# Optimization experiments

Hardware: AMD Instinct MI355X
Metric: run time of the kernel (lower is better)

The kernel has to match this reference:

```python
import jax, jax.numpy as jnp
import numpy as np

THRESHOLD = 0.5  # args.threshold: mask prob >= threshold means 'read' this token
HIDDEN = 256
EMBED = 300
BATCH = 64
STEPS = 2048


def setup_inputs() -> dict:
    key = jax.random.key(0)
    ks = jax.random.split(key, 10)
    H, E = HIDDEN, EMBED
    s = 1.0 / np.sqrt(H)
    return {
        "embedded": jax.random.normal(ks[0], (BATCH, STEPS, E), dtype=jnp.float32),
        "mask": jax.random.uniform(ks[1], (BATCH, STEPS), dtype=jnp.float32),
        "lengths": jax.random.randint(ks[2], (BATCH,), 1, STEPS + 1),
        # LSTM cell params (torch gate order i, f, g, o)
        "W_ih": jax.random.uniform(ks[3], (4 * H, E), minval=-s, maxval=s, dtype=jnp.float32),
        "W_hh": jax.random.uniform(ks[4], (4 * H, H), minval=-s, maxval=s, dtype=jnp.float32),
        "b_ih": jax.random.uniform(ks[5], (4 * H,), minval=-s, maxval=s, dtype=jnp.float32),
        "b_hh": jax.random.uniform(ks[6], (4 * H,), minval=-s, maxval=s, dtype=jnp.float32),
        "W_out": jax.random.uniform(ks[7], (2, H), minval=-s, maxval=s, dtype=jnp.float32),
        "b_out": jax.random.uniform(ks[8], (2,), minval=-s, maxval=s, dtype=jnp.float32),
    }


def reference(embedded, mask, lengths, W_ih, W_hh, b_ih, b_hh, W_out, b_out):
    B, T, E = embedded.shape
    H = W_hh.shape[1]
    b = b_ih + b_hh

    def step(carry, xs):
        h, c = carry
        x_t, m_t = xs  # [B,E], [B]
        z = x_t @ W_ih.T + h @ W_hh.T + b  # [B,4H]
        i, f, g, o = jnp.split(z, 4, axis=-1)
        i = jax.nn.sigmoid(i)
        f = jax.nn.sigmoid(f)
        g = jnp.tanh(g)
        o = jax.nn.sigmoid(o)
        c_new = f * c + i * g
        h_new = o * jnp.tanh(c_new)
        read = (m_t >= THRESHOLD)[:, None]  # skip-RNN gate
        h2 = jnp.where(read, h_new, h)
        c2 = jnp.where(read, c_new, c)
        return (h2, c2), h2

    h0 = jnp.zeros((B, H), embedded.dtype)
    c0 = jnp.zeros((B, H), embedded.dtype)
    xs = (jnp.swapaxes(embedded, 0, 1), mask.T)  # time-major
    _, hs = jax.lax.scan(step, (h0, c0), xs)  # hs: [T,B,H]

    idx = jnp.clip(lengths - 1, 0, T - 1)
    last = hs[idx, jnp.arange(B)]  # [B,H] last relevant output
    logits = last @ W_out.T + b_out
    probs = jax.nn.softmax(logits, axis=-1)
    predictions = jnp.argmax(probs, axis=1)
    return probs, predictions
```

## Files before the change

### kernel.cpp

```cpp
#include <hip/hip_runtime.h>
#include <math.h>

#define BATCH  64
#define TSTEPS 2048
#define EMBED  300
#define HID    256
#define GATES  1024
#define WSTRIDE 34
#define ASTR   328

typedef __fp16 h2 __attribute__((ext_vector_type(2)));
typedef __fp16 h4 __attribute__((ext_vector_type(4)));
typedef __fp16 h8 __attribute__((ext_vector_type(8)));
typedef float  f4 __attribute__((ext_vector_type(4)));

__device__ __forceinline__ h2 pack_h2(float a, float b) {
    return __builtin_amdgcn_cvt_pkrtz(a, b);
}
__device__ __forceinline__ h2 bc_h2(unsigned u) {
    return __builtin_bit_cast(h2, u);
}
__device__ __forceinline__ float dot2f(h2 w, h2 h, float acc) {
#if __has_builtin(__builtin_amdgcn_fdot2)
    return __builtin_amdgcn_fdot2(w, h, acc, false);
#else
    return acc + (float)w[0]*(float)h[0] + (float)w[1]*(float)h[1];
#endif
}
__device__ __forceinline__ float rcpf_(float x) {
#if __has_builtin(__builtin_amdgcn_rcpf)
    return __builtin_amdgcn_rcpf(x);
#else
    return 1.0f / x;
#endif
}
__device__ __forceinline__ float sigm_(float x) { return rcpf_(1.f + __expf(-x)); }
__device__ __forceinline__ float tanh_(float x) { return 1.f - 2.f*rcpf_(__expf(2.f*x) + 1.f); }

__global__ __launch_bounds__(256) void k_compact(
    const float* __restrict__ mask, const int* __restrict__ lengths,
    int* __restrict__ list, int* __restrict__ cnt,
    float* __restrict__ h_state, float* __restrict__ c_state,
    int t0, int CT, int first_chunk)
{
    int b = blockIdx.x, tid = threadIdx.x;
    if (first_chunk) {
        h_state[b*HID + tid] = 0.f;
        c_state[b*HID + tid] = 0.f;
    }
    int idx = lengths[b] - 1;
    idx = idx < 0 ? 0 : (idx > TSTEPS-1 ? TSTEPS-1 : idx);

    __shared__ int wcnt[4];
    __shared__ int running;
    if (tid == 0) running = 0;
    __syncthreads();

    for (int base = 0; base < CT; base += 256) {
        int t = t0 + base + tid;
        bool pred = ((base + tid) < CT) && (t <= idx)
                    && (mask[b*TSTEPS + t] >= 0.5f);
        unsigned long long bal = __ballot(pred);
        int wave = tid >> 6, lane = tid & 63;
        if (lane == 0) wcnt[wave] = __popcll(bal);
        __syncthreads();
        int off = running;
        for (int w2 = 0; w2 < wave; ++w2) off += wcnt[w2];
        off += __popcll(bal & ((1ull << lane) - 1ull));
        if (pred) list[b*CT + off] = t;
        __syncthreads();
        if (tid == 0) running += wcnt[0] + wcnt[1] + wcnt[2] + wcnt[3];
        __syncthreads();
    }
    if (tid == 0) cnt[b] = running;
}

__global__ __launch_bounds__(256) void k_gemm(
    const float* __restrict__ emb, const float* __restrict__ W_ih,
    const int* __restrict__ list, const int* __restrict__ cnt,
    float* __restrict__ Z, int CT)
{
    int b = blockIdx.z;
    int mb = cnt[b];
    int n0 = blockIdx.x * 128;
    int tid = threadIdx.x;
    int w = tid >> 6, l = tid & 63;

    __shared__ _Float16 Al[64 * ASTR];
    __shared__ _Float16 Bl[128 * ASTR];
    __shared__ int tl[64];

    for (int idx = tid; idx < 128*75; idx += 256) {
        int r = idx / 75, c = idx - 75*r;
        float4 v = ((const float4*)(W_ih + (size_t)(n0 + r)*EMBED))[c];
        *(h2*)&Bl[r*ASTR + 4*c]     = pack_h2(v.x, v.y);
        *(h2*)&Bl[r*ASTR + 4*c + 2] = pack_h2(v.z, v.w);
    }
    for (int idx = tid; idx < 128*14; idx += 256) {
        int r = idx / 14, c2 = idx - 14*r;
        *(unsigned*)&Bl[r*ASTR + 300 + 2*c2] = 0u;
    }
    for (int idx = tid; idx < 64*14; idx += 256) {
        int r = idx / 14, c2 = idx - 14*r;
        *(unsigned*)&Al[r*ASTR + 300 + 2*c2] = 0u;
    }

    int arow = w*16 + (l & 15);
    int kg4  = (l >> 4) * 4;
    int drow0 = w*16 + (l >> 4)*4;

    for (int i0 = 0; i0 < mb; i0 += 64) {
        __syncthreads();
        if (tid < 64) {
            int j = i0 + tid;
            tl[tid] = (j < mb) ? list[b*CT + j] : -1;
        }
        __syncthreads();
        for (int idx = tid; idx < 64*75; idx += 256) {
            int r = idx / 75, c = idx - 75*r;
            float4 v = {0.f, 0.f, 0.f, 0.f};
            int trow = tl[r];
            if (trow >= 0)
                v = ((const float4*)(emb + ((size_t)b*TSTEPS + trow)*EMBED))[c];
            *(h2*)&Al[r*ASTR + 4*c]     = pack_h2(v.x, v.y);
            *(h2*)&Al[r*ASTR + 4*c + 2] = pack_h2(v.z, v.w);
        }
        __syncthreads();

        f4 acc[8];
        #pragma unroll
        for (int nt = 0; nt < 8; ++nt) acc[nt] = f4{0.f, 0.f, 0.f, 0.f};

        #pragma unroll 2
        for (int ks = 0; ks < 10; ++ks) {
            int kb = ks*32 + kg4;
            h4 alo = *(const h4*)&Al[arow*ASTR + kb];
            h4 ahi = *(const h4*)&Al[arow*ASTR + kb + 16];
            h8 af = __builtin_shufflevector(alo, ahi, 0,1,2,3,4,5,6,7);
            #pragma unroll
            for (int nt = 0; nt < 8; ++nt) {
                int brow = nt*16 + (l & 15);
                h4 blo = *(const h4*)&Bl[brow*ASTR + kb];
                h4 bhi = *(const h4*)&Bl[brow*ASTR + kb + 16];
                h8 bf = __builtin_shufflevector(blo, bhi, 0,1,2,3,4,5,6,7);
                acc[nt] = __builtin_amdgcn_mfma_f32_16x16x32_f16(af, bf, acc[nt], 0, 0, 0);
            }
        }

        #pragma unroll
        for (int nt = 0; nt < 8; ++nt) {
            #pragma unroll
            for (int j = 0; j < 4; ++j) {
                int r = drow0 + j;
                if (i0 + r < mb)
                    Z[((size_t)b*CT + i0 + r)*GATES + n0 + nt*16 + (l & 15)] = acc[nt][j];
            }
        }
    }
}

__global__ __launch_bounds__(1024, 1) void k_lstm(
    const float* __restrict__ Z, const int* __restrict__ cnt,
    const float* __restrict__ W_hh,
    const float* __restrict__ b_ih, const float* __restrict__ b_hh,
    float* __restrict__ h_state, float* __restrict__ c_state, int CT)
{
    int b = blockIdx.x;
    int tid = threadIdx.x;
    int d   = tid & 255;
    int g   = tid >> 8;

    __shared__ unsigned wlds[1024 * WSTRIDE];
    __shared__ float act3[3][256];
    __shared__ __align__(16) _Float16 h_arr[HID];

    for (int idx = tid; idx < 1024*32; idx += 1024) {
        int r = idx >> 5, k = idx & 31;
        float2 v = ((const float2*)(W_hh + (size_t)r*HID))[k];
        *(h2*)&wlds[r*WSTRIDE + k] = pack_h2(v.x, v.y);
    }
    h2 wr[96];
    {
        const float2* pw = (const float2*)(W_hh + (size_t)tid*HID);
        #pragma unroll
        for (int t = 0; t < 96; ++t) {
            float2 v = pw[32 + t];
            wr[t] = pack_h2(v.x, v.y);
        }
    }
    float bias = b_ih[tid] + b_hh[tid];

    float c_reg = 0.f;
    if (tid < 256) {
        h_arr[d] = (_Float16)h_state[(size_t)b*HID + d];
        c_reg    = c_state[(size_t)b*HID + d];
    }
    __syncthreads();

    int mb = cnt[b];
    float zcur = (mb > 0) ? Z[((size_t)b*CT)*GATES + tid] : 0.f;

    for (int j = 0; j < mb; ++j) {
        float znext = (j + 1 < mb) ? Z[((size_t)b*CT + j + 1)*GATES + tid] : 0.f;

        float a0 = 0.f, a1 = 0.f;
        #pragma unroll
        for (int c = 0; c < 32; ++c) {
            uint4 hv = ((const uint4*)h_arr)[c];
            h2 h0 = bc_h2(hv.x), h1 = bc_h2(hv.y);
            h2 hx = bc_h2(hv.z), h3 = bc_h2(hv.w);
            h2 w0, w1, w2, w3;
            if (c < 8) {
                uint2 q01 = *(const uint2*)&wlds[tid*WSTRIDE + 4*c];
                uint2 q23 = *(const uint2*)&wlds[tid*WSTRIDE + 4*c + 2];
                w0 = bc_h2(q01.x); w1 = bc_h2(q01.y);
                w2 = bc_h2(q23.x); w3 = bc_h2(q23.y);
            } else {
                int t = (c - 8) * 4;
                w0 = wr[t+0]; w1 = wr[t+1]; w2 = wr[t+2]; w3 = wr[t+3];
            }
            a0 = dot2f(w0, h0, a0);
            a1 = dot2f(w1, h1, a1);
            a0 = dot2f(w2, hx, a0);
            a1 = dot2f(w3, h3, a1);
        }
        float a = zcur + bias + (a0 + a1);
        float v = (g == 2) ? tanh_(a) : sigm_(a);
        if (g) act3[g-1][d] = v;
        __syncthreads();

        if (tid < 256) {
            float fv = act3[0][d], gv = act3[1][d], ov = act3[2][d];
            c_reg = fv * c_reg + v * gv;
            float hn = ov * tanh_(c_reg);
            h_arr[d] = (_Float16)hn;
        }
        __syncthreads();
        zcur = znext;
    }

    if (tid < 256) {
        h_state[(size_t)b*HID + d] = (float)h_arr[d];
        c_state[(size_t)b*HID + d] = c_reg;
    }
}

__global__ __launch_bounds__(64) void k_final(
    const float* __restrict__ h_state, const float* __restrict__ W_out,
    const float* __restrict__ b_out, float* __restrict__ out)
{
    int b = threadIdx.x;
    float l0 = b_out[0], l1 = b_out[1];
    for (int k = 0; k < HID; ++k) {
        float h = h_state[b*HID + k];
        l0 += h * W_out[k];
        l1 += h * W_out[HID + k];
    }
    float m  = fmaxf(l0, l1);
    float e0 = expf(l0 - m), e1 = expf(l1 - m);
    float s  = e0 + e1;
    float p0 = e0 / s, p1 = e1 / s;
    out[b*2 + 0] = p0;
    out[b*2 + 1] = p1;
    out[BATCH*2 + b] = (p1 > p0) ? 1.0f : 0.0f;
}

extern "C" void kernel_launch(void* const* d_in, const int* in_sizes, int n_in,
                              void* d_out, int out_size, void* d_ws, size_t ws_size,
                              hipStream_t stream)
{
    (void)in_sizes; (void)n_in; (void)out_size;
    const float* emb   = (const float*)d_in[0];
    const float* mask  = (const float*)d_in[1];
    const int*   len   = (const int*)  d_in[2];
    const float* W_ih  = (const float*)d_in[3];
    const float* W_hh  = (const float*)d_in[4];
    const float* b_ih  = (const float*)d_in[5];
    const float* b_hh  = (const float*)d_in[6];
    const float* W_out = (const float*)d_in[7];
    const float* b_out = (const float*)d_in[8];
    float* out = (float*)d_out;

    char* p = (char*)d_ws;
    auto carve = [&](size_t bytes) -> char* {
        char* r = p;
        p += (bytes + 255) & ~(size_t)255;
        return r;
    };
    float* h_state = (float*)carve((size_t)BATCH*HID*4);
    float* c_state = (float*)carve((size_t)BATCH*HID*4);
    int*   cntb    = (int*)  carve((size_t)BATCH*4);

    size_t fixed = (size_t)(p - (char*)d_ws);
    int CT = TSTEPS;
    while (CT > 64) {
        size_t lb = (((size_t)BATCH*CT*4) + 255) & ~(size_t)255;
        size_t zb = (size_t)BATCH*CT*GATES*4;
        if (fixed + lb + zb + 1024 <= ws_size) break;
        CT >>= 1;
    }
    int*   list = (int*)  carve((size_t)BATCH*CT*4);
    float* Z    = (float*)carve((size_t)BATCH*CT*GATES*4);

    int nchunks = TSTEPS / CT;
    for (int c = 0; c < nchunks; ++c) {
        int t0 = c * CT;
        int first = (c == 0) ? 1 : 0;
        hipLaunchKernelGGL(k_compact, dim3(BATCH), dim3(256), 0, stream,
                           mask, len, list, cntb, h_state, c_state,
                           t0, CT, first);
        hipLaunchKernelGGL(k_gemm, dim3(8, 1, BATCH), dim3(256), 0, stream,
                           emb, W_ih, list, cntb, Z, CT);
        hipLaunchKernelGGL(k_lstm, dim3(BATCH), dim3(1024), 0, stream,
                           Z, cntb, W_hh, b_ih, b_hh,
                           h_state, c_state, CT);
    }
    hipLaunchKernelGGL(k_final, dim3(1), dim3(64), 0, stream,
                       h_state, W_out, b_out, out);
}
```

Baseline: 2.579 ms.

## Compute LSTM recurrent matvec with MFMA using register-resident W_hh fragments

The recurrent h·W_hh product in the per-batch LSTM kernel now runs as MFMA 16x16x32 f16 instructions instead of per-thread fdot2 loops. The whole fp16 W_hh slice is held in registers as MFMA B-fragments, and only row 0 of the A operand carries h (other lanes are masked to zero). The block shrinks from 1024 to 512 threads, and the 256 cell threads each apply all four gates, removing the separate activation exchange array. Most of each MFMA's work is wasted on zero rows, and holding 64 h8 fragments per thread puts heavy pressure on registers.

After: 4.995 ms. 93.7% more time.

```diff
diff --git a/kernel.cpp b/kernel.cpp
--- a/kernel.cpp
+++ b/kernel.cpp
@@ -6,7 +6,6 @@
 #define EMBED  300
 #define HID    256
 #define GATES  1024
-#define WSTRIDE 34
 #define ASTR   328
 
 typedef __fp16 h2 __attribute__((ext_vector_type(2)));
@@ -17,15 +16,8 @@
 __device__ __forceinline__ h2 pack_h2(float a, float b) {
     return __builtin_amdgcn_cvt_pkrtz(a, b);
 }
-__device__ __forceinline__ h2 bc_h2(unsigned u) {
-    return __builtin_bit_cast(h2, u);
-}
-__device__ __forceinline__ float dot2f(h2 w, h2 h, float acc) {
-#if __has_builtin(__builtin_amdgcn_fdot2)
-    return __builtin_amdgcn_fdot2(w, h, acc, false);
-#else
-    return acc + (float)w[0]*(float)h[0] + (float)w[1]*(float)h[1];
-#endif
+__device__ __forceinline__ unsigned pack_u(float a, float b) {
+    return __builtin_bit_cast(unsigned, __builtin_amdgcn_cvt_pkrtz(a, b));
 }
 __device__ __forceinline__ float rcpf_(float x) {
 #if __has_builtin(__builtin_amdgcn_rcpf)
@@ -93,8 +85,8 @@
     for (int idx = tid; idx < 128*75; idx += 256) {
         int r = idx / 75, c = idx - 75*r;
         float4 v = ((const float4*)(W_ih + (size_t)(n0 + r)*EMBED))[c];
-        *(h2*)&Bl[r*ASTR + 4*c]     = pack_h2(v.x, v.y);
-        *(h2*)&Bl[r*ASTR + 4*c + 2] = pack_h2(v.z, v.w);
+        *(unsigned*)&Bl[r*ASTR + 4*c]     = pack_u(v.x, v.y);
+        *(unsigned*)&Bl[r*ASTR + 4*c + 2] = pack_u(v.z, v.w);
     }
     for (int idx = tid; idx < 128*14; idx += 256) {
         int r = idx / 14, c2 = idx - 14*r;
@@ -122,8 +114,8 @@
             int trow = tl[r];
             if (trow >= 0)
                 v = ((const float4*)(emb + ((size_t)b*TSTEPS + trow)*EMBED))[c];
-            *(h2*)&Al[r*ASTR + 4*c]     = pack_h2(v.x, v.y);
-            *(h2*)&Al[r*ASTR + 4*c + 2] = pack_h2(v.z, v.w);
+            *(unsigned*)&Al[r*ASTR + 4*c]     = pack_u(v.x, v.y);
+            *(unsigned*)&Al[r*ASTR + 4*c + 2] = pack_u(v.z, v.w);
         }
         __syncthreads();
 
@@ -159,84 +151,103 @@
     }
 }
 
-__global__ __launch_bounds__(1024, 1) void k_lstm(
+__global__ __launch_bounds__(512) void k_lstm(
     const float* __restrict__ Z, const int* __restrict__ cnt,
     const float* __restrict__ W_hh,
     const float* __restrict__ b_ih, const float* __restrict__ b_hh,
     float* __restrict__ h_state, float* __restrict__ c_state, int CT)
 {
-    int b = blockIdx.x;
+    int b   = blockIdx.x;
     int tid = threadIdx.x;
+    int w   = tid >> 6;
+    int l   = tid & 63;
+    int g   = l >> 4;
+    int cl  = l & 15;
     int d   = tid & 255;
-    int g   = tid >> 8;
-
-    __shared__ unsigned wlds[1024 * WSTRIDE];
-    __shared__ float act3[3][256];
+
     __shared__ __align__(16) _Float16 h_arr[HID];
-
-    for (int idx = tid; idx < 1024*32; idx += 1024) {
-        int r = idx >> 5, k = idx & 31;
-        float2 v = ((const float2*)(W_hh + (size_t)r*HID))[k];
-        *(h2*)&wlds[r*WSTRIDE + k] = pack_h2(v.x, v.y);
-    }
-    h2 wr[96];
-    {
-        const float2* pw = (const float2*)(W_hh + (size_t)tid*HID);
+    __shared__ float yl[GATES];
+
+    h8 wb[64];
+    #pragma unroll
+    for (int f = 0; f < 64; ++f) {
+        int nt = f >> 3, ks = f & 7;
+        int row = 128*w + 16*nt + cl;
+        const float* src = W_hh + (size_t)row*HID + ks*32 + 4*g;
+        float4 lo = *(const float4*)src;
+        float4 hi = *(const float4*)(src + 16);
+        uint4 uu;
+        uu.x = pack_u(lo.x, lo.y);
+        uu.y = pack_u(lo.z, lo.w);
+        uu.z = pack_u(hi.x, hi.y);
+        uu.w = pack_u(hi.z, hi.w);
+        wb[f] = __builtin_bit_cast(h8, uu);
+    }
+
+    float c_reg = 0.f, bI = 0.f, bF = 0.f, bG = 0.f, bO = 0.f;
+    if (tid < 256) {
+        c_reg = c_state[(size_t)b*HID + d];
+        h_arr[d] = (_Float16)h_state[(size_t)b*HID + d];
+        bI = b_ih[d]       + b_hh[d];
+        bF = b_ih[256 + d] + b_hh[256 + d];
+        bG = b_ih[512 + d] + b_hh[512 + d];
+        bO = b_ih[768 + d] + b_hh[768 + d];
+    }
+    __syncthreads();
+
+    int mb = cnt[b];
+    float zI = 0.f, zF = 0.f, zG = 0.f, zO = 0.f;
+    if (mb > 0 && tid < 256) {
+        const float* zr = Z + ((size_t)b*CT)*GATES;
+        zI = zr[d]; zF = zr[256 + d]; zG = zr[512 + d]; zO = zr[768 + d];
+    }
+    unsigned amask = (cl == 0) ? 0xFFFFFFFFu : 0u;
+
+    for (int j = 0; j < mb; ++j) {
+        float zIn = 0.f, zFn = 0.f, zGn = 0.f, zOn = 0.f;
+        if (j + 1 < mb && tid < 256) {
+            const float* zr = Z + ((size_t)b*CT + j + 1)*GATES;
+            zIn = zr[d]; zFn = zr[256 + d]; zGn = zr[512 + d]; zOn = zr[768 + d];
+        }
+
+        f4 acc[8];
         #pragma unroll
-        for (int t = 0; t < 96; ++t) {
-            float2 v = pw[32 + t];
-            wr[t] = pack_h2(v.x, v.y);
-        }
-    }
-    float bias = b_ih[tid] + b_hh[tid];
-
-    float c_reg = 0.f;
-    if (tid < 256) {
-        h_arr[d] = (_Float16)h_state[(size_t)b*HID + d];
-        c_reg    = c_state[(size_t)b*HID + d];
-    }
-    __syncthreads();
-
-    int mb = cnt[b];
-    float zcur = (mb > 0) ? Z[((size_t)b*CT)*GATES + tid] : 0.f;
-
-    for (int j = 0; j < mb; ++j) {
-        float znext = (j + 1 < mb) ? Z[((size_t)b*CT + j + 1)*GATES + tid] : 0.f;
-
-        float a0 = 0.f, a1 = 0.f;
+        for (int nt = 0; nt < 8; ++nt) acc[nt] = f4{0.f, 0.f, 0.f, 0.f};
+
         #pragma unroll
-        for (int c = 0; c < 32; ++c) {
-            uint4 hv = ((const uint4*)h_arr)[c];
-            h2 h0 = bc_h2(hv.x), h1 = bc_h2(hv.y);
-            h2 hx = bc_h2(hv.z), h3 = bc_h2(hv.w);
-            h2 w0, w1, w2, w3;
-            if (c < 8) {
-                uint2 q01 = *(const uint2*)&wlds[tid*WSTRIDE + 4*c];
-                uint2 q23 = *(const uint2*)&wlds[tid*WSTRIDE + 4*c + 2];
-                w0 = bc_h2(q01.x); w1 = bc_h2(q01.y);
-                w2 = bc_h2(q23.x); w3 = bc_h2(q23.y);
-            } else {
-                int t = (c - 8) * 4;
-                w0 = wr[t+0]; w1 = wr[t+1]; w2 = wr[t+2]; w3 = wr[t+3];
-            }
-            a0 = dot2f(w0, h0, a0);
-            a1 = dot2f(w1, h1, a1);
-            a0 = dot2f(w2, hx, a0);
-            a1 = dot2f(w3, h3, a1);
-        }
-        float a = zcur + bias + (a0 + a1);
-        float v = (g == 2) ? tanh_(a) : sigm_(a);
-        if (g) act3[g-1][d] = v;
+        for (int ks = 0; ks < 8; ++ks) {
+            int k0 = ks*32 + 4*g;
+            uint2 ha = *(const uint2*)&h_arr[k0];
+            uint2 hb = *(const uint2*)&h_arr[k0 + 16];
+            uint4 ua;
+            ua.x = ha.x & amask; ua.y = ha.y & amask;
+            ua.z = hb.x & amask; ua.w = hb.y & amask;
+            h8 af = __builtin_bit_cast(h8, ua);
+            #pragma unroll
+            for (int nt = 0; nt < 8; ++nt)
+                acc[nt] = __builtin_amdgcn_mfma_f32_16x16x32_f16(af, wb[nt*8 + ks], acc[nt], 0, 0, 0);
+        }
+
+        if (l < 16) {
+            #pragma unroll
+            for (int nt = 0; nt < 8; ++nt)
+                yl[128*w + 16*nt + l] = acc[nt][0];
+        }
         __syncthreads();
 
         if (tid < 256) {
-            float fv = act3[0][d], gv = act3[1][d], ov = act3[2][d];
-            c_reg = fv * c_reg + v * gv;
+            float aI = yl[d]       + zI + bI;
+            float aF = yl[256 + d] + zF + bF;
+            float aG = yl[512 + d] + zG + bG;
+            float aO = yl[768 + d] + zO + bO;
+            float iv = sigm_(aI), fv = sigm_(aF);
+            float gv = tanh_(aG), ov = sigm_(aO);
+            c_reg = fv * c_reg + iv * gv;
             float hn = ov * tanh_(c_reg);
             h_arr[d] = (_Float16)hn;
         }
         __syncthreads();
-        zcur = znext;
+        zI = zIn; zF = zFn; zG = zGn; zO = zOn;
     }
 
     if (tid < 256) {
@@ -311,7 +322,7 @@
                            t0, CT, first);
         hipLaunchKernelGGL(k_gemm, dim3(8, 1, BATCH), dim3(256), 0, stream,
                            emb, W_ih, list, cntb, Z, CT);
-        hipLaunchKernelGGL(k_lstm, dim3(BATCH), dim3(1024), 0, stream,
+        hipLaunchKernelGGL(k_lstm, dim3(BATCH), dim3(512), 0, stream,
                            Z, cntb, W_hh, b_ih, b_hh,
                            h_state, c_state, CT);
     }
```
